# Performance work log

Hardware: AMD Instinct MI355X
Metric: run time of the kernel (lower is better)

The kernel has to match this reference:

```python
import jax, jax.numpy as jnp
import numpy as np

SS, D, V = 64, 256, 10000
B, S = 16, 512


def setup_inputs() -> dict:
    key = jax.random.key(0)
    ks = jax.random.split(key, 7)
    scale = lambda fan_in: 1.0 / np.sqrt(fan_in)
    return {
        "x": jax.random.normal(ks[0], (B, S, D), dtype=jnp.float32),
        # nn.Linear(D, 4*ss): weight [4ss, D], bias [4ss]
        "Wxs_w": jax.random.uniform(ks[1], (4 * SS, D), jnp.float32, -scale(D), scale(D)),
        "Wxs_b": jax.random.uniform(ks[2], (4 * SS,), jnp.float32, -scale(D), scale(D)),
        # nn.Linear(ss, 4*ss)
        "Wss_w": jax.random.uniform(ks[3], (4 * SS, SS), jnp.float32, -scale(SS), scale(SS)),
        "Wss_b": jax.random.uniform(ks[4], (4 * SS,), jnp.float32, -scale(SS), scale(SS)),
        # nn.Linear(ss, V)
        "Wsy_w": jax.random.uniform(ks[5], (V, SS), jnp.float32, -scale(SS), scale(SS)),
        "Wsy_b": jax.random.uniform(ks[6], (V,), jnp.float32, -scale(SS), scale(SS)),
    }


def reference(x, Wxs_w, Wxs_b, Wss_w, Wss_b, Wsy_w, Wsy_b):
    b, s, _ = x.shape
    ss = Wss_w.shape[1]
    # Precompute input projections for all timesteps: [s, b, 4ss]
    xproj = jnp.einsum("bsd,kd->sbk", x, Wxs_w) + Wxs_b

    def step(carry, xp_t):
        h, c = carry
        comb = xp_t + h @ Wss_w.T + Wss_b  # [b, 4ss]
        f, i, g, o = jnp.split(comb, 4, axis=-1)
        f = jax.nn.sigmoid(f)
        i = jax.nn.sigmoid(i)
        o = jax.nn.sigmoid(o)
        g = jnp.tanh(g)
        c = c * f + i * g
        h = o * c  # NOTE: original code omits tanh(c) here; stay faithful
        return (h, c), h

    h0 = jnp.zeros((b, ss), dtype=x.dtype)
    c0 = jnp.zeros((b, ss), dtype=x.dtype)
    _, hs = jax.lax.scan(step, (h0, c0), xproj)  # hs: [s, b, ss]
    # Per-step vocab projection == batched projection of stacked hidden states
    y = jnp.einsum("sbh,vh->bsv", hs, Wsy_w) + Wsy_b  # [b, s, V]
    return y
```

## Files before the change

kernel.cpp:

```cpp
#include <hip/hip_runtime.h>

typedef unsigned short u16;
typedef unsigned int u32;

using short8 = __attribute__((ext_vector_type(8))) short;
using f32x4  = __attribute__((ext_vector_type(4))) float;
using f32x2  = __attribute__((ext_vector_type(2))) float;

#define SSEQ 512
#define BB   16
#define DD   256
#define G4   256
#define SSZ  64
#define VV   10000
#define VPAD 10112
#define MALL 8192

#define OFF_XHI   0u
#define OFF_XLO   4194304u
#define OFF_WHI   8388608u
#define OFF_WLO   8519680u
#define OFF_WSY   8650752u
#define OFF_XPROJ 9945088u
#define OFF_HS    18333696u
#define OFF_PROG  19382272u

__device__ __forceinline__ u16 f2bf(float f) {
  u32 u = __float_as_uint(f);
  u32 r = (u + 0x7fffu + ((u >> 16) & 1u)) >> 16;
  return (u16)r;
}
__device__ __forceinline__ float bf2f(u16 h) {
  return __uint_as_float(((u32)h) << 16);
}
__device__ __forceinline__ f32x2 pkfma(f32x2 a, f32x2 b, f32x2 c) {
  asm("v_pk_fma_f32 %0, %1, %2, %0" : "+v"(c) : "v"(a), "v"(b));
  return c;
}
template <int CTRL>
__device__ __forceinline__ float qadd(float x) {
  int pv = __builtin_amdgcn_update_dpp(0, __float_as_int(x), CTRL, 0xf, 0xf, true);
  return x + __int_as_float(pv);
}
template <int CTRL>
__device__ __forceinline__ float qbcast(float x) {
  int pv = __builtin_amdgcn_update_dpp(0, __float_as_int(x), CTRL, 0xf, 0xf, true);
  return __int_as_float(pv);
}

#define NX 2097152
#define NW 65536
#define NP 647168
__global__ void k0_convert(const float* __restrict__ x, const float* __restrict__ Wxs,
                           const float* __restrict__ Wsy,
                           u16* __restrict__ xhi, u16* __restrict__ xlo,
                           u16* __restrict__ whi, u16* __restrict__ wlo,
                           u16* __restrict__ wsyb, int* __restrict__ prog) {
  int i = blockIdx.x * 256 + threadIdx.x;
  if (i < NX) {
    float v = x[i]; u16 h = f2bf(v);
    xhi[i] = h; xlo[i] = f2bf(v - bf2f(h));
  } else if (i < NX + NW) {
    int j = i - NX;
    float v = Wxs[j]; u16 h = f2bf(v);
    whi[j] = h; wlo[j] = f2bf(v - bf2f(h));
  } else if (i < NX + NW + NP) {
    int j = i - NX - NW;
    wsyb[j] = (j < VV * SSZ) ? f2bf(Wsy[j]) : (u16)0;
  } else {
    int j = i - NX - NW - NP;
    if (j < BB)
      __hip_atomic_store(prog + j, 0, __ATOMIC_RELEASE, __HIP_MEMORY_SCOPE_AGENT);
  }
}

__global__ __launch_bounds__(256) void k1_xproj(
    const u16* __restrict__ xhi, const u16* __restrict__ xlo,
    const u16* __restrict__ whi, const u16* __restrict__ wlo,
    const float* __restrict__ bias, float* __restrict__ xproj) {
  int bid = blockIdx.x;
  int mb = bid >> 1, nb = bid & 1;
  int tid = threadIdx.x, l = tid & 63, wid = tid >> 6;
  int wm = wid >> 1, wv = wid & 1;
  int m0 = mb * 128 + wm * 64, n0 = nb * 128 + wv * 64;
  int lr = l & 15, lg = l >> 4;

  f32x4 acc[4][4];
#pragma unroll
  for (int a = 0; a < 4; a++)
#pragma unroll
    for (int bq = 0; bq < 4; bq++) acc[a][bq] = (f32x4){0.f, 0.f, 0.f, 0.f};

#pragma unroll
  for (int p = 0; p < 3; p++) {
    const u16* A = (p == 1) ? xlo : xhi;
    const u16* B = (p == 2) ? wlo : whi;
#pragma unroll
    for (int ks = 0; ks < 8; ks++) {
      short8 af[4], bf_[4];
#pragma unroll
      for (int fm = 0; fm < 4; fm++)
        af[fm] = *(const short8*)(A + (size_t)(m0 + fm * 16 + lr) * 256 + ks * 32 + lg * 8);
#pragma unroll
      for (int fv = 0; fv < 4; fv++)
        bf_[fv] = *(const short8*)(B + (size_t)(n0 + fv * 16 + lr) * 256 + ks * 32 + lg * 8);
#pragma unroll
      for (int fm = 0; fm < 4; fm++)
#pragma unroll
        for (int fv = 0; fv < 4; fv++)
          acc[fm][fv] = __builtin_amdgcn_mfma_f32_16x16x32_bf16(af[fm], bf_[fv], acc[fm][fv], 0, 0, 0);
    }
  }
#pragma unroll
  for (int fv = 0; fv < 4; fv++) {
    int j = n0 + fv * 16 + lr;
    float bj = bias[j];
#pragma unroll
    for (int fm = 0; fm < 4; fm++)
#pragma unroll
      for (int r = 0; r < 4; r++) {
        int m = m0 + fm * 16 + lg * 4 + r;
        xproj[(size_t)m * 256 + j] = acc[fm][fv][r] + bj;
      }
  }
}

__global__ __launch_bounds__(256, 1) void k23_fused(
    const float* __restrict__ xproj, const float* __restrict__ Wss,
    const float* __restrict__ Wssb, u16* __restrict__ hsb,
    const u16* __restrict__ wsyb, const float* __restrict__ ybias,
    float* __restrict__ y, int* __restrict__ prog) {
  __shared__ float hbuf[2][64];
  int bid = blockIdx.x, tid = threadIdx.x;

  if (bid < BB) {
    int b = bid;
    int w = tid >> 6, l = tid & 63;
    int oo = l >> 2, ks = l & 3;
    int jj = w * 16 + oo;
    int ks16 = ks * 16;

    f32x2 wr[32];
#pragma unroll
    for (int g = 0; g < 4; g++) {
      const f32x2* pw = (const f32x2*)(Wss + (size_t)(g * 64 + jj) * 64 + ks16);
#pragma unroll
      for (int q = 0; q < 8; q++) wr[g * 8 + q] = pw[q];
    }
    float mybias = Wssb[ks * 64 + jj];

    float kk = (ks == 2) ? 2.885390082f : -1.442695041f;
    float Ac = (ks == 2) ? 1.f : 0.f;
    float Bc = (ks == 2) ? -2.f : 1.f;

    const float* xqp = xproj + (size_t)b * SSEQ * 256 + ks * 64 + jj;
    float xs0 = xqp[0 * 256];
    float xs1 = xqp[1 * 256];
    float xs2 = xqp[2 * 256];
    float xs3 = xqp[3 * 256];

    u16* hout = hsb + (size_t)b * SSEQ * 64 + jj;

    if (tid < 128) ((float*)hbuf)[tid] = 0.f;
    __syncthreads();

    float c = 0.f;

#define STEP(T, XS, RB, WB) { \
    f32x4 h4[4]; \
    const f32x4* hb = (const f32x4*)&hbuf[RB][ks16]; \
    h4[0] = hb[0]; h4[1] = hb[1]; h4[2] = hb[2]; h4[3] = hb[3]; \
    float p[4]; \
    _Pragma("unroll") \
    for (int g = 0; g < 4; g++) { \
      f32x2 a0 = (f32x2){0.f, 0.f}, a1 = (f32x2){0.f, 0.f}; \
      _Pragma("unroll") \
      for (int q = 0; q < 4; q++) { \
        f32x2 hA = (f32x2){h4[q][0], h4[q][1]}; \
        f32x2 hB = (f32x2){h4[q][2], h4[q][3]}; \
        a0 = pkfma(hA, wr[g * 8 + 2 * q], a0); \
        a1 = pkfma(hB, wr[g * 8 + 2 * q + 1], a1); \
      } \
      f32x2 ps = a0 + a1; \
      p[g] = ps[0] + ps[1]; \
    } \
    _Pragma("unroll") \
    for (int g = 0; g < 4; g++) p[g] = qadd<0x4E>(qadd<0xB1>(p[g])); \
    float myp = (ks == 1) ? p[1] : p[0]; \
    myp = (ks == 2) ? p[2] : myp; \
    myp = (ks == 3) ? p[3] : myp; \
    float aa = myp + XS + mybias; \
    if ((T) + 4 < SSEQ) XS = xqp[(size_t)((T) + 4) * 256]; \
    float z = exp2f(kk * aa); \
    float act = fmaf(Bc, __builtin_amdgcn_rcpf(z + 1.f), Ac); \
    float fg = qbcast<0x00>(act); \
    float ig = qbcast<0x55>(act); \
    float gg = qbcast<0xAA>(act); \
    float og = qbcast<0xFF>(act); \
    c = fmaf(c, fg, ig * gg); \
    float hn = og * c;   \
    if (ks == 0) { \
      hbuf[WB][jj] = hn; \
      __builtin_nontemporal_store(f2bf(hn), hout + (size_t)(T) * 64); \
    } \
    asm volatile("s_waitcnt lgkmcnt(0)\n\ts_barrier" ::: "memory"); \
  }

    for (int t = 0; t < SSEQ; t += 32) {
#pragma unroll
      for (int tq = 0; tq < 32; tq += 4) {
        STEP(t + tq + 0, xs0, 1, 0)
        STEP(t + tq + 1, xs1, 0, 1)
        STEP(t + tq + 2, xs2, 1, 0)
        STEP(t + tq + 3, xs3, 0, 1)
      }
      asm volatile("s_waitcnt vmcnt(0)" ::: "memory");
      __syncthreads();
      if (tid == 0)
        __hip_atomic_store(prog + b, t + 32, __ATOMIC_RELEASE, __HIP_MEMORY_SCOPE_AGENT);
    }
#undef STEP
  } else {
    int gb = bid - BB;
    int l = tid & 63, wid = tid >> 6;
    int wm = wid >> 1, wv = wid & 1;
    int lr = l & 15, lg = l >> 4;

    for (int idx = gb; idx < 4 * BB * 79; idx += 256 - BB) {
      int tb = idx / (BB * 79);
      int rem = idx - tb * BB * 79;
      int b = rem / 79;
      int vb = rem - b * 79;
      int need = tb * 128 + 128;

      while (__hip_atomic_load(prog + b, __ATOMIC_RELAXED, __HIP_MEMORY_SCOPE_AGENT) < need)
        __builtin_amdgcn_s_sleep(32);
      __builtin_amdgcn_fence(__ATOMIC_ACQUIRE, "agent");

      int m0 = b * SSEQ + tb * 128 + wm * 64;
      int v0 = vb * 128 + wv * 64;

      f32x4 acc[4][4];
#pragma unroll
      for (int a = 0; a < 4; a++)
#pragma unroll
        for (int bq = 0; bq < 4; bq++) acc[a][bq] = (f32x4){0.f, 0.f, 0.f, 0.f};

#pragma unroll
      for (int ks = 0; ks < 2; ks++) {
        short8 af[4], bf_[4];
#pragma unroll
        for (int fm = 0; fm < 4; fm++)
          af[fm] = *(const short8*)(hsb + (size_t)(m0 + fm * 16 + lr) * 64 + ks * 32 + lg * 8);
#pragma unroll
        for (int fv = 0; fv < 4; fv++)
          bf_[fv] = *(const short8*)(wsyb + (size_t)(v0 + fv * 16 + lr) * 64 + ks * 32 + lg * 8);
#pragma unroll
        for (int fv = 0; fv < 4; fv++)
#pragma unroll
          for (int fm = 0; fm < 4; fm++)
            acc[fv][fm] = __builtin_amdgcn_mfma_f32_16x16x32_bf16(bf_[fv], af[fm], acc[fv][fm], 0, 0, 0);
      }

#pragma unroll
      for (int fv = 0; fv < 4; fv++) {
        int vb4 = v0 + fv * 16 + lg * 4;
        bool ok = (vb4 + 3) < VV;
        float4 bv = ok ? *(const float4*)(ybias + vb4) : float4{0.f, 0.f, 0.f, 0.f};
#pragma unroll
        for (int fm = 0; fm < 4; fm++) {
          int m = m0 + fm * 16 + lr;
          if (ok) {
            float4 o;
            o.x = acc[fv][fm][0] + bv.x;
            o.y = acc[fv][fm][1] + bv.y;
            o.z = acc[fv][fm][2] + bv.z;
            o.w = acc[fv][fm][3] + bv.w;
            *(float4*)(y + (size_t)m * (size_t)VV + vb4) = o;
          }
        }
      }
    }
  }
}

extern "C" void kernel_launch(void* const* d_in, const int* in_sizes, int n_in,
                              void* d_out, int out_size, void* d_ws, size_t ws_size,
                              hipStream_t stream) {
  const float* x     = (const float*)d_in[0];
  const float* Wxs_w = (const float*)d_in[1];
  const float* Wxs_b = (const float*)d_in[2];
  const float* Wss_w = (const float*)d_in[3];
  const float* Wss_b = (const float*)d_in[4];
  const float* Wsy_w = (const float*)d_in[5];
  const float* Wsy_b = (const float*)d_in[6];
  float* y = (float*)d_out;
  char* ws = (char*)d_ws;

  u16*   xhi   = (u16*)(ws + OFF_XHI);
  u16*   xlo   = (u16*)(ws + OFF_XLO);
  u16*   whi   = (u16*)(ws + OFF_WHI);
  u16*   wlo   = (u16*)(ws + OFF_WLO);
  u16*   wsyb  = (u16*)(ws + OFF_WSY);
  float* xproj = (float*)(ws + OFF_XPROJ);
  u16*   hsb   = (u16*)(ws + OFF_HS);
  int*   prog  = (int*)(ws + OFF_PROG);

  k0_convert<<<(NX + NW + NP) / 256 + 1, 256, 0, stream>>>(
      x, Wxs_w, Wsy_w, xhi, xlo, whi, wlo, wsyb, prog);
  k1_xproj<<<128, 256, 0, stream>>>(xhi, xlo, whi, wlo, Wxs_b, xproj);
  k23_fused<<<256, 256, 0, stream>>>(xproj, Wss_w, Wss_b, hsb, wsyb, Wsy_b, y, prog);
}
```

Measured before the change: 290.1 us.

## Shrink projection tiles to 32 timesteps and deepen xproj prefetch to 8

The consumer blocks now process the vocab projection in 32-row time tiles instead of 128, so they can start once the recurrence publishes each 32-step chunk. This gives finer-grained overlap with the sequential LSTM. Each warp now computes a 16x64 tile instead of 64x64, which lowers MFMA reuse per weight load and means more reloads of Wsy fragments. The recurrence also prefetches xproj 8 steps ahead instead of 4, and the spin-wait sleep is shortened.

```diff
diff --git a/kernel.cpp b/kernel.cpp
--- a/kernel.cpp
+++ b/kernel.cpp
@@ -158,6 +158,10 @@
     float xs1 = xqp[1 * 256];
     float xs2 = xqp[2 * 256];
     float xs3 = xqp[3 * 256];
+    float xs4 = xqp[4 * 256];
+    float xs5 = xqp[5 * 256];
+    float xs6 = xqp[6 * 256];
+    float xs7 = xqp[7 * 256];
 
     u16* hout = hsb + (size_t)b * SSEQ * 64 + jj;
 
@@ -190,7 +194,7 @@
     myp = (ks == 2) ? p[2] : myp; \
     myp = (ks == 3) ? p[3] : myp; \
     float aa = myp + XS + mybias; \
-    if ((T) + 4 < SSEQ) XS = xqp[(size_t)((T) + 4) * 256]; \
+    if ((T) + 8 < SSEQ) XS = xqp[(size_t)((T) + 8) * 256]; \
     float z = exp2f(kk * aa); \
     float act = fmaf(Bc, __builtin_amdgcn_rcpf(z + 1.f), Ac); \
     float fg = qbcast<0x00>(act); \
@@ -208,11 +212,15 @@
 
     for (int t = 0; t < SSEQ; t += 32) {
 #pragma unroll
-      for (int tq = 0; tq < 32; tq += 4) {
+      for (int tq = 0; tq < 32; tq += 8) {
         STEP(t + tq + 0, xs0, 1, 0)
         STEP(t + tq + 1, xs1, 0, 1)
         STEP(t + tq + 2, xs2, 1, 0)
         STEP(t + tq + 3, xs3, 0, 1)
+        STEP(t + tq + 4, xs4, 1, 0)
+        STEP(t + tq + 5, xs5, 0, 1)
+        STEP(t + tq + 6, xs6, 1, 0)
+        STEP(t + tq + 7, xs7, 0, 1)
       }
       asm volatile("s_waitcnt vmcnt(0)" ::: "memory");
       __syncthreads();
@@ -226,40 +234,34 @@
     int wm = wid >> 1, wv = wid & 1;
     int lr = l & 15, lg = l >> 4;
 
-    for (int idx = gb; idx < 4 * BB * 79; idx += 256 - BB) {
-      int tb = idx / (BB * 79);
-      int rem = idx - tb * BB * 79;
+    for (int idx = gb; idx < 16 * BB * 79; idx += 256 - BB) {
+      int lvl = idx / (BB * 79);
+      int rem = idx - lvl * (BB * 79);
       int b = rem / 79;
       int vb = rem - b * 79;
-      int need = tb * 128 + 128;
+      int need = lvl * 32 + 32;
 
       while (__hip_atomic_load(prog + b, __ATOMIC_RELAXED, __HIP_MEMORY_SCOPE_AGENT) < need)
-        __builtin_amdgcn_s_sleep(32);
+        __builtin_amdgcn_s_sleep(8);
       __builtin_amdgcn_fence(__ATOMIC_ACQUIRE, "agent");
 
-      int m0 = b * SSEQ + tb * 128 + wm * 64;
+      int m0 = b * SSEQ + lvl * 32 + wm * 16;
       int v0 = vb * 128 + wv * 64;
 
-      f32x4 acc[4][4];
-#pragma unroll
-      for (int a = 0; a < 4; a++)
-#pragma unroll
-        for (int bq = 0; bq < 4; bq++) acc[a][bq] = (f32x4){0.f, 0.f, 0.f, 0.f};
+      f32x4 acc[4];
+#pragma unroll
+      for (int a = 0; a < 4; a++) acc[a] = (f32x4){0.f, 0.f, 0.f, 0.f};
 
 #pragma unroll
       for (int ks = 0; ks < 2; ks++) {
-        short8 af[4], bf_[4];
-#pragma unroll
-        for (int fm = 0; fm < 4; fm++)
-          af[fm] = *(const short8*)(hsb + (size_t)(m0 + fm * 16 + lr) * 64 + ks * 32 + lg * 8);
+        short8 af = *(const short8*)(hsb + (size_t)(m0 + lr) * 64 + ks * 32 + lg * 8);
+        short8 bf_[4];
 #pragma unroll
         for (int fv = 0; fv < 4; fv++)
           bf_[fv] = *(const short8*)(wsyb + (size_t)(v0 + fv * 16 + lr) * 64 + ks * 32 + lg * 8);
 #pragma unroll
         for (int fv = 0; fv < 4; fv++)
-#pragma unroll
-          for (int fm = 0; fm < 4; fm++)
-            acc[fv][fm] = __builtin_amdgcn_mfma_f32_16x16x32_bf16(bf_[fv], af[fm], acc[fv][fm], 0, 0, 0);
+          acc[fv] = __builtin_amdgcn_mfma_f32_16x16x32_bf16(bf_[fv], af, acc[fv], 0, 0, 0);
       }
 
 #pragma unroll
@@ -267,17 +269,14 @@
         int vb4 = v0 + fv * 16 + lg * 4;
         bool ok = (vb4 + 3) < VV;
         float4 bv = ok ? *(const float4*)(ybias + vb4) : float4{0.f, 0.f, 0.f, 0.f};
-#pragma unroll
-        for (int fm = 0; fm < 4; fm++) {
-          int m = m0 + fm * 16 + lr;
-          if (ok) {
-            float4 o;
-            o.x = acc[fv][fm][0] + bv.x;
-            o.y = acc[fv][fm][1] + bv.y;
-            o.z = acc[fv][fm][2] + bv.z;
-            o.w = acc[fv][fm][3] + bv.w;
-            *(float4*)(y + (size_t)m * (size_t)VV + vb4) = o;
-          }
+        int m = m0 + lr;
+        if (ok) {
+          float4 o;
+          o.x = acc[fv][0] + bv.x;
+          o.y = acc[fv][1] + bv.y;
+          o.z = acc[fv][2] + bv.z;
+          o.w = acc[fv][3] + bv.w;
+          *(float4*)(y + (size_t)m * (size_t)VV + vb4) = o;
         }
       }
     }
```

New measurement: 690.4 us. 138% more time.
